# Kernel tuning notes

Hardware: AMD Instinct MI355X
Metric: run time of the kernel (lower is better)

## Reference

```python
import jax, jax.numpy as jnp
import numpy as np

# Static graph layout: 64 equal-size graphs so per-graph k is static (jit-friendly).
B = 64          # number of graphs
N_PER = 4096    # nodes per graph (batch vector is sorted, equal blocks)
N = B * N_PER   # 262144 total nodes
C = 128         # in_channels
E = 4194304     # number of edges (avg degree 16)
RATIO = 0.8
K = int(np.ceil(RATIO * N_PER))  # 3277 nodes kept per graph


def setup_inputs() -> dict:
    key = jax.random.key(0)
    k1, k2, k3 = jax.random.split(key, 3)
    x = jax.random.normal(k1, (N, C), dtype=jnp.float32)
    # learned projection (torch init is zeros; use small randn so scores are non-degenerate)
    coefficient = jax.random.normal(k2, (C, 1), dtype=jnp.float32) * 0.1
    edge_index = jax.random.randint(k3, (2, E), 0, N, dtype=jnp.int32)
    # sorted, equal-size graph assignment (matches torch_geometric batch convention)
    batch = jnp.repeat(jnp.arange(B, dtype=jnp.int32), N_PER)
    return {"x": x, "coefficient": coefficient, "edge_index": edge_index, "batch": batch}


def reference(x, coefficient, edge_index, batch):
    # score = x @ coefficient, squeezed -> [N]
    score = (x @ coefficient)[:, 0]

    # topk(): per-graph descending sort + take top ceil(ratio*n) nodes.
    # Equal-size sorted graphs -> dense view is a plain reshape; lax.top_k gives
    # descending-sorted indices per graph, matching torch's dense sort+mask path.
    dense = score.reshape(B, N_PER)              # [B, N_PER]
    _, idx = jax.lax.top_k(dense, K)             # [B, K] local indices, score-descending
    offsets = (jnp.arange(B, dtype=idx.dtype) * N_PER)[:, None]
    perm = (idx + offsets).reshape(-1)           # [B*K] global node indices

    # gather nodes, gate by sigmoid(score)
    gate = jax.nn.sigmoid(score[perm])           # [B*K]
    x_pooled = x[perm] * gate[:, None]           # [B*K, C]
    batch_pooled = batch[perm]

    # filter_adj: relabel kept nodes 0..B*K-1, drop edges with a removed endpoint.
    node_map = jnp.full((N,), -1, dtype=jnp.int32)
    node_map = node_map.at[perm].set(jnp.arange(perm.shape[0], dtype=jnp.int32))
    row = node_map[edge_index[0]]
    col = node_map[edge_index[1]]
    valid = (row >= 0) & (col >= 0)              # [E]
    # static-shape equivalent of torch's dynamic edge filtering: stable-sort valid
    # edges to the front (preserving original order), pad invalid slots with -1.
    order = jnp.argsort(jnp.logical_not(valid), stable=True)
    new_edge_index = jnp.stack([row, col])[:, order]
    new_edge_index = jnp.where(valid[order][None, :], new_edge_index, -1)

    return (x_pooled, new_edge_index, batch_pooled, perm)
```

## Files before the change

### kernel.cpp

```cpp
#include <hip/hip_runtime.h>
#include <hip/hip_bf16.h>

#define BG    64
#define NPER  4096
#define NTOT  (BG * NPER)
#define CC    128
#define EE    4194304
#define KK    3277
#define BK    (BG * KK)
#define NBLK  512
#define EPB   8192

#define OFF_X     0
#define OFF_EDGE  (BK * CC)
#define OFF_BATCH (OFF_EDGE + 2 * EE)
#define OFF_PERM  (OFF_BATCH + BK)

#define CH0_BYTES  ((size_t)OFF_EDGE * 4)
#define A_OFF_B    (CH0_BYTES - (size_t)NTOT * 4)
#define BM_OFF_B   (A_OFF_B - 32768)
#define LP_OFF_B   (BM_OFF_B - 16384)
#define BO_OFF_B   (LP_OFF_B - 8192)
#define BC_OFF_B   (LP_OFF_B - 16384)
#define CTRL_OFF_B (LP_OFF_B - 16640)
#define PAIRS_OFF_B (CTRL_OFF_B - (size_t)EE * 4)

typedef unsigned long long u64;

static __device__ __forceinline__ unsigned short bf16_bits(float f) {
    __hip_bfloat16 h = __float2bfloat16(f);
    return *reinterpret_cast<unsigned short*>(&h);
}
static __device__ __forceinline__ unsigned obf(float v) {
    return ((unsigned)bf16_bits(v)) << 16;
}
static __device__ __forceinline__ unsigned ald(const unsigned* p) {
    return __hip_atomic_load(p, __ATOMIC_ACQUIRE, __HIP_MEMORY_SCOPE_AGENT);
}
static __device__ __forceinline__ void ast(unsigned* p, unsigned v) {
    __hip_atomic_store(p, v, __ATOMIC_RELEASE, __HIP_MEMORY_SCOPE_AGENT);
}

__global__ void score_kernel(const float* __restrict__ x,
                             const float* __restrict__ coef,
                             float* __restrict__ arr_f,
                             unsigned* __restrict__ ctrl) {
    if (blockIdx.x == 0 && threadIdx.x < 2) ast(&ctrl[threadIdx.x], 0u);

    int lane = threadIdx.x & 63;
    int half = lane >> 5;
    int cg   = lane & 31;
    int waveId = (blockIdx.x * blockDim.x + threadIdx.x) >> 6;
    int nWaves = (gridDim.x * blockDim.x) >> 6;

    float4 c = ((const float4*)coef)[cg];

    for (int pair = waveId; pair < NTOT / 2; pair += nWaves) {
        int row = 2 * pair + half;
        float4 v = ((const float4*)(x + (size_t)row * CC))[cg];
        double s = (double)v.x * c.x + (double)v.y * c.y
                 + (double)v.z * c.z + (double)v.w * c.w;
        #pragma unroll
        for (int off = 16; off > 0; off >>= 1)
            s += __shfl_xor(s, off, 64);
        if (cg == 0) arr_f[row] = (float)s;
    }
}

__global__ __launch_bounds__(512) void topk_kernel(const float* __restrict__ arr_f,
                                                   unsigned* __restrict__ st_li,
                                                   unsigned* __restrict__ st_gate,
                                                   unsigned* __restrict__ bm_g,
                                                   unsigned short* __restrict__ lp_g) {
    __shared__ unsigned hist[2048];
    __shared__ unsigned sScan[512];
    __shared__ unsigned sSel[2];
    __shared__ unsigned sTie[128];
    __shared__ unsigned lbm[128];
    __shared__ unsigned lpc[128];

    int b = blockIdx.x, t = threadIdx.x;
    const float* s = arr_f + (b << 12);

    float4 v0 = *(const float4*)(s + (t << 3));
    float4 v1 = *(const float4*)(s + (t << 3) + 4);
    float vv[8] = {v0.x, v0.y, v0.z, v0.w, v1.x, v1.y, v1.z, v1.w};
    unsigned key[8];
    #pragma unroll
    for (int m = 0; m < 8; ++m) {
        unsigned u = __float_as_uint(vv[m]);
        u = u ^ ((u >> 31) ? 0xFFFFFFFFu : 0x80000000u);
        key[m] = ~u;
    }

    unsigned need = KK;

    for (int i = t; i < 2048; i += 512) hist[i] = 0;
    __syncthreads();
    #pragma unroll
    for (int m = 0; m < 8; ++m) atomicAdd(&hist[key[m] >> 21], 1u);
    __syncthreads();
    {
        unsigned c0 = hist[t*4], c1 = hist[t*4+1], c2 = hist[t*4+2], c3 = hist[t*4+3];
        unsigned s4 = c0 + c1 + c2 + c3;
        sScan[t] = s4; __syncthreads();
        #pragma unroll
        for (int off = 1; off < 512; off <<= 1) {
            unsigned add = (t >= off) ? sScan[t-off] : 0u; __syncthreads();
            sScan[t] += add; __syncthreads();
        }
        unsigned excl = sScan[t] - s4;
        if (excl < need && need <= sScan[t]) {
            unsigned cum = excl, bin = t*4u;
            if      (cum + c0 >= need)           { sSel[0]=bin;   sSel[1]=cum; }
            else if (cum + c0 + c1 >= need)      { sSel[0]=bin+1; sSel[1]=cum+c0; }
            else if (cum + c0 + c1 + c2 >= need) { sSel[0]=bin+2; sSel[1]=cum+c0+c1; }
            else                                 { sSel[0]=bin+3; sSel[1]=cum+c0+c1+c2; }
        }
        __syncthreads();
    }
    unsigned B1 = sSel[0]; need -= sSel[1];
    __syncthreads();

    for (int i = t; i < 2048; i += 512) hist[i] = 0;
    __syncthreads();
    #pragma unroll
    for (int m = 0; m < 8; ++m)
        if ((key[m] >> 21) == B1) atomicAdd(&hist[(key[m] >> 10) & 2047u], 1u);
    __syncthreads();
    {
        unsigned c0 = hist[t*4], c1 = hist[t*4+1], c2 = hist[t*4+2], c3 = hist[t*4+3];
        unsigned s4 = c0 + c1 + c2 + c3;
        sScan[t] = s4; __syncthreads();
        #pragma unroll
        for (int off = 1; off < 512; off <<= 1) {
            unsigned add = (t >= off) ? sScan[t-off] : 0u; __syncthreads();
            sScan[t] += add; __syncthreads();
        }
        unsigned excl = sScan[t] - s4;
        if (excl < need && need <= sScan[t]) {
            unsigned cum = excl, bin = t*4u;
            if      (cum + c0 >= need)           { sSel[0]=bin;   sSel[1]=cum; }
            else if (cum + c0 + c1 >= need)      { sSel[0]=bin+1; sSel[1]=cum+c0; }
            else if (cum + c0 + c1 + c2 >= need) { sSel[0]=bin+2; sSel[1]=cum+c0+c1; }
            else                                 { sSel[0]=bin+3; sSel[1]=cum+c0+c1+c2; }
        }
        __syncthreads();
    }
    unsigned B2 = sSel[0]; need -= sSel[1];
    unsigned P2 = (B1 << 11) | B2;
    __syncthreads();

    for (int i = t; i < 2048; i += 512) hist[i] = 0;
    __syncthreads();
    #pragma unroll
    for (int m = 0; m < 8; ++m)
        if ((key[m] >> 10) == P2) atomicAdd(&hist[key[m] & 1023u], 1u);
    __syncthreads();
    {
        unsigned c0 = hist[t*2], c1 = hist[t*2+1];
        unsigned s2 = c0 + c1;
        sScan[t] = s2; __syncthreads();
        #pragma unroll
        for (int off = 1; off < 512; off <<= 1) {
            unsigned add = (t >= off) ? sScan[t-off] : 0u; __syncthreads();
            sScan[t] += add; __syncthreads();
        }
        unsigned excl = sScan[t] - s2;
        if (excl < need && need <= sScan[t]) {
            if (excl + c0 >= need) { sSel[0] = t*2u;   sSel[1] = excl; }
            else                   { sSel[0] = t*2u+1; sSel[1] = excl + c0; }
        }
        __syncthreads();
    }
    unsigned KSTAR = (P2 << 10) | sSel[0];
    unsigned needT = need - sSel[1];
    __syncthreads();

    if (t < 128) sTie[t] = 0;
    __syncthreads();
    #pragma unroll
    for (int m = 0; m < 8; ++m) {
        if (key[m] == KSTAR) {
            unsigned idx = (unsigned)((t << 3) | m);
            atomicOr(&sTie[idx >> 5], 1u << (idx & 31));
        }
    }
    __syncthreads();
    if (t == 0) {
        unsigned rem = needT, it = 0;
        for (int w = 0; w < 128; ++w) {
            unsigned word = sTie[w], pc = __popc(word);
            if (rem <= pc) {
                for (unsigned bit = 0; ; ++bit)
                    if ((word >> bit) & 1u) { if (--rem == 0) { it = w*32u + bit; break; } }
                break;
            }
            rem -= pc;
        }
        sSel[0] = it;
    }
    __syncthreads();
    unsigned idxT = sSel[0];

    if (t < 128) lbm[t] = 0u;
    __syncthreads();
    unsigned kmask = 0;
    #pragma unroll
    for (int m = 0; m < 8; ++m) {
        unsigned idx = (unsigned)((t << 3) | m);
        bool kept = (key[m] < KSTAR) || (key[m] == KSTAR && idx <= idxT);
        if (kept) { kmask |= 1u << m; atomicOr(&lbm[idx >> 5], 1u << (idx & 31)); }
    }
    __syncthreads();
    if (t < 128) lpc[t] = __popc(lbm[t]);
    __syncthreads();
    #pragma unroll
    for (int off = 1; off < 128; off <<= 1) {
        unsigned add = (t < 128 && t >= off) ? lpc[t - off] : 0u;
        __syncthreads();
        if (t < 128) lpc[t] += add;
        __syncthreads();
    }
    if (t < 128) {
        unsigned w = lbm[t];
        bm_g[(b << 7) + t] = w;
        lp_g[(b << 7) + t] = (unsigned short)(lpc[t] - __popc(w));
    }
    #pragma unroll
    for (int m = 0; m < 8; ++m) {
        if ((kmask >> m) & 1u) {
            unsigned idx = (unsigned)((t << 3) | m);
            unsigned w = lbm[idx >> 5];
            unsigned p = (lpc[idx >> 5] - __popc(w))
                       + (unsigned)__popc(w & ((1u << (idx & 31)) - 1u));
            int j = b * KK + (int)p;
            float gate = 1.0f / (1.0f + expf(-vv[m]));
            st_li[j]   = idx;
            st_gate[j] = __float_as_uint(gate);
        }
    }
}

__global__ __launch_bounds__(512, 4) void edge_pass1(
        const int* __restrict__ edge,
        const unsigned* __restrict__ bm_g,
        const unsigned short* __restrict__ lp_g,
        unsigned* __restrict__ pairs,
        unsigned* __restrict__ counts,
        unsigned* __restrict__ prefix,
        unsigned* __restrict__ ctrl) {
    __shared__ unsigned sBm[8192];
    __shared__ unsigned short sLp[8192];
    __shared__ unsigned sWaveSum[8];
    __shared__ unsigned sScan[512];
    __shared__ int sTicket;

    int b = blockIdx.x;
    int base = b << 13;
    int tid = threadIdx.x;
    int lane = tid & 63, wid = tid >> 6;
    u64 lmask = (1ull << lane) - 1ull;

    {
        const uint4* bmv = (const uint4*)bm_g;
        uint4* sBmv = (uint4*)sBm;
        #pragma unroll
        for (int r = 0; r < 4; ++r) sBmv[(r << 9) + tid] = bmv[(r << 9) + tid];
        const uint4* lpv = (const uint4*)lp_g;
        uint4* sLpv = (uint4*)sLp;
        #pragma unroll
        for (int r = 0; r < 2; ++r) sLpv[(r << 9) + tid] = lpv[(r << 9) + tid];
    }
    __syncthreads();

    int chunk = base + (wid << 10);

    int ev0[16], ev1[16];
    #pragma unroll
    for (int k = 0; k < 16; ++k) ev0[k] = edge[chunk + (k << 6) + lane];
    #pragma unroll
    for (int k = 0; k < 16; ++k) ev1[k] = edge[EE + chunk + (k << 6) + lane];

    u64 bal[16];
    unsigned pk[16];
    unsigned cnt = 0;
    #pragma unroll
    for (int k = 0; k < 16; ++k) {
        int u0i = ev0[k], u1i = ev1[k];
        unsigned w0 = sBm[u0i >> 5], w1 = sBm[u1i >> 5];
        bool valid = ((w0 >> (u0i & 31)) & (w1 >> (u1i & 31)) & 1u) != 0u;
        bal[k] = __ballot(valid);
        unsigned pkk = 0;
        if (valid) {
            unsigned j0 = (unsigned)(u0i >> 12) * KK + sLp[u0i >> 5]
                        + (unsigned)__popc(w0 & ((1u << (u0i & 31)) - 1u));
            unsigned j1 = (unsigned)(u1i >> 12) * KK + sLp[u1i >> 5]
                        + (unsigned)__popc(w1 & ((1u << (u1i & 31)) - 1u));
            pkk = obf((float)j0) | (unsigned)bf16_bits((float)j1);
        }
        pk[k] = pkk;
        cnt += (unsigned)__popcll(bal[k]);
    }

    if (lane == 0) sWaveSum[wid] = cnt;
    __syncthreads();

    unsigned waveBase = 0, run = 0;
    #pragma unroll
    for (int w = 0; w < 8; ++w) {
        unsigned s = sWaveSum[w];
        if (w < wid) waveBase += s;
        run += s;
    }

    unsigned* pb = pairs + base;
    unsigned wrun = 0;
    #pragma unroll
    for (int k = 0; k < 16; ++k) {
        if ((bal[k] >> lane) & 1ull) {
            unsigned pos = waveBase + wrun + (unsigned)__popcll(bal[k] & lmask);
            pb[pos] = pk[k];
        }
        wrun += (unsigned)__popcll(bal[k]);
    }

    if (tid == 0) {
        ast(&counts[b], run);
        sTicket = (int)__hip_atomic_fetch_add(&ctrl[0], 1u, __ATOMIC_ACQ_REL,
                                              __HIP_MEMORY_SCOPE_AGENT);
    }
    __syncthreads();

    if (sTicket == NBLK - 1) {
        unsigned v = ald(&counts[tid]);
        sScan[tid] = v;
        __syncthreads();
        #pragma unroll
        for (int off = 1; off < 512; off <<= 1) {
            unsigned add = (tid >= off) ? sScan[tid - off] : 0u;
            __syncthreads();
            sScan[tid] += add;
            __syncthreads();
        }
        prefix[tid] = sScan[tid] - v;
        if (tid == 511) prefix[NBLK] = sScan[511];
    }
}

__global__ __launch_bounds__(256) void edge_pass2(
        const unsigned* __restrict__ pairs,
        const unsigned* __restrict__ prefix,
        unsigned* __restrict__ out32) {
    int b = blockIdx.x;
    unsigned base = (unsigned)(b << 13);
    unsigned tid = threadIdx.x;
    unsigned blockOff = prefix[b];
    unsigned cnt = prefix[b + 1] - blockOff;
    unsigned nvalid = prefix[NBLK];
    unsigned* oe = out32 + OFF_EDGE;
    const unsigned* pb = pairs + base;

    for (unsigned i = tid; i < cnt; i += 256u) {
        unsigned w = pb[i];
        oe[blockOff + i]      = w & 0xFFFF0000u;
        oe[EE + blockOff + i] = w << 16;
    }
    unsigned tailBase = nvalid + base - blockOff;
    unsigned tcnt = (unsigned)EPB - cnt;
    unsigned NEG1 = obf(-1.0f);
    for (unsigned i = tid; i < tcnt; i += 256u) {
        oe[tailBase + i]      = NEG1;
        oe[EE + tailBase + i] = NEG1;
    }
}

__global__ void gather_kernel(const float* __restrict__ x,
                              const unsigned* __restrict__ st_li,
                              const unsigned* __restrict__ st_gate,
                              unsigned* __restrict__ out32) {
    int tid = blockIdx.x * blockDim.x + threadIdx.x;
    int rowsPerGrid = (gridDim.x * blockDim.x) >> 5;
    int rid = tid >> 5;
    int cg  = tid & 31;

    for (int row = rid; row < BK; row += rowsPerGrid) {
        int b  = row / KK;
        int li = (int)st_li[row];
        int node = (b << 12) + li;
        float g = __uint_as_float(st_gate[row]);
        float4 v = ((const float4*)(x + (size_t)node * CC))[cg];
        uint4 o;
        o.x = obf(v.x * g);
        o.y = obf(v.y * g);
        o.z = obf(v.z * g);
        o.w = obf(v.w * g);
        ((uint4*)(out32 + OFF_X))[(size_t)row * 32 + cg] = o;
        if (cg == 0) {
            out32[OFF_BATCH + row] = obf((float)b);
            out32[OFF_PERM + row]  = obf((float)node);
        }
    }
}

extern "C" void kernel_launch(void* const* d_in, const int* in_sizes, int n_in,
                              void* d_out, int out_size, void* d_ws, size_t ws_size,
                              hipStream_t stream) {
    const float* x    = nullptr;
    const float* coef = nullptr;
    const int*   edge = nullptr;
    for (int i = 0; i < n_in; ++i) {
        switch (in_sizes[i]) {
            case NTOT * CC: x    = (const float*)d_in[i]; break;
            case CC:        coef = (const float*)d_in[i]; break;
            case 2 * EE:    edge = (const int*)d_in[i];   break;
            default: break;
        }
    }
    if (!x || !coef || !edge) return;

    char* ob = (char*)d_out;
    unsigned* out32 = (unsigned*)d_out;
    float*          A      = (float*)(ob + A_OFF_B);
    unsigned*       bm_g   = (unsigned*)(ob + BM_OFF_B);
    unsigned short* lp_g   = (unsigned short*)(ob + LP_OFF_B);
    unsigned*       counts = (unsigned*)(ob + BC_OFF_B);
    unsigned*       prefix = (unsigned*)(ob + BO_OFF_B);
    unsigned*       ctrl   = (unsigned*)(ob + CTRL_OFF_B);
    unsigned*       pairs  = (unsigned*)(ob + PAIRS_OFF_B);
    unsigned* st_li   = out32 + OFF_BATCH;
    unsigned* st_gate = out32 + OFF_PERM;

    score_kernel<<<2048, 256, 0, stream>>>(x, coef, A, ctrl);
    topk_kernel<<<BG, 512, 0, stream>>>(A, st_li, st_gate, bm_g, lp_g);
    edge_pass1<<<NBLK, 512, 0, stream>>>(edge, bm_g, lp_g, pairs, counts,
                                         prefix, ctrl);
    edge_pass2<<<NBLK, 256, 0, stream>>>(pairs, prefix, out32);
    gather_kernel<<<4096, 256, 0, stream>>>(x, st_li, st_gate, out32);
}
```

Measured before the change: 139.4 us.

## Move scratch buffers to workspace and fuse edge pass2 with gather kernel

Scratch buffers (scores, bitmaps, pairs, counts, prefix, ctrl) move from the output buffer into the workspace when it is large enough. That removes the overlap between the scratch areas and the output regions. With the overlap gone, edge_pass2 and the gather kernel become independent and are merged into one launch with disjoint block ranges, so edge compaction and row gathering run concurrently and one launch is saved. If no workspace is available, the old two-launch path is used.

```diff
diff --git a/kernel.cpp b/kernel.cpp
--- a/kernel.cpp
+++ b/kernel.cpp
@@ -24,6 +24,15 @@
 #define BC_OFF_B   (LP_OFF_B - 16384)
 #define CTRL_OFF_B (LP_OFF_B - 16640)
 #define PAIRS_OFF_B (CTRL_OFF_B - (size_t)EE * 4)
+
+#define WS_PAIRS_B  ((size_t)0)
+#define WS_A_B      ((size_t)EE * 4)
+#define WS_BM_B     (WS_A_B + (size_t)NTOT * 4)
+#define WS_LP_B     (WS_BM_B + 32768)
+#define WS_BC_B     (WS_LP_B + 16384)
+#define WS_BO_B     (WS_BC_B + 2048)
+#define WS_CTRL_B   (WS_BO_B + 2064)
+#define WS_NEEDED   (WS_CTRL_B + 16)
 
 typedef unsigned long long u64;
 
@@ -348,13 +357,12 @@
     }
 }
 
-__global__ __launch_bounds__(256) void edge_pass2(
+static __device__ __forceinline__ void pass2_body(
+        int b, unsigned tid,
         const unsigned* __restrict__ pairs,
         const unsigned* __restrict__ prefix,
         unsigned* __restrict__ out32) {
-    int b = blockIdx.x;
     unsigned base = (unsigned)(b << 13);
-    unsigned tid = threadIdx.x;
     unsigned blockOff = prefix[b];
     unsigned cnt = prefix[b + 1] - blockOff;
     unsigned nvalid = prefix[NBLK];
@@ -375,14 +383,14 @@
     }
 }
 
-__global__ void gather_kernel(const float* __restrict__ x,
-                              const unsigned* __restrict__ st_li,
-                              const unsigned* __restrict__ st_gate,
-                              unsigned* __restrict__ out32) {
-    int tid = blockIdx.x * blockDim.x + threadIdx.x;
-    int rowsPerGrid = (gridDim.x * blockDim.x) >> 5;
-    int rid = tid >> 5;
-    int cg  = tid & 31;
+static __device__ __forceinline__ void gather_body(
+        int gtid, int rowsPerGrid,
+        const float* __restrict__ x,
+        const unsigned* __restrict__ st_li,
+        const unsigned* __restrict__ st_gate,
+        unsigned* __restrict__ out32) {
+    int rid = gtid >> 5;
+    int cg  = gtid & 31;
 
     for (int row = rid; row < BK; row += rowsPerGrid) {
         int b  = row / KK;
@@ -403,6 +411,36 @@
     }
 }
 
+__global__ __launch_bounds__(256) void fused_p2_gather(
+        const unsigned* __restrict__ pairs,
+        const unsigned* __restrict__ prefix,
+        const float* __restrict__ x,
+        const unsigned* __restrict__ st_li,
+        const unsigned* __restrict__ st_gate,
+        unsigned* __restrict__ out32) {
+    if (blockIdx.x < NBLK) {
+        pass2_body(blockIdx.x, threadIdx.x, pairs, prefix, out32);
+    } else {
+        int gtid = (blockIdx.x - NBLK) * 256 + threadIdx.x;
+        gather_body(gtid, (4096 * 256) >> 5, x, st_li, st_gate, out32);
+    }
+}
+
+__global__ __launch_bounds__(256) void edge_pass2(
+        const unsigned* __restrict__ pairs,
+        const unsigned* __restrict__ prefix,
+        unsigned* __restrict__ out32) {
+    pass2_body(blockIdx.x, threadIdx.x, pairs, prefix, out32);
+}
+
+__global__ void gather_kernel(const float* __restrict__ x,
+                              const unsigned* __restrict__ st_li,
+                              const unsigned* __restrict__ st_gate,
+                              unsigned* __restrict__ out32) {
+    int gtid = blockIdx.x * blockDim.x + threadIdx.x;
+    gather_body(gtid, (int)((gridDim.x * blockDim.x) >> 5), x, st_li, st_gate, out32);
+}
+
 extern "C" void kernel_launch(void* const* d_in, const int* in_sizes, int n_in,
                               void* d_out, int out_size, void* d_ws, size_t ws_size,
                               hipStream_t stream) {
@@ -419,22 +457,30 @@
     }
     if (!x || !coef || !edge) return;
 
-    char* ob = (char*)d_out;
     unsigned* out32 = (unsigned*)d_out;
-    float*          A      = (float*)(ob + A_OFF_B);
-    unsigned*       bm_g   = (unsigned*)(ob + BM_OFF_B);
-    unsigned short* lp_g   = (unsigned short*)(ob + LP_OFF_B);
-    unsigned*       counts = (unsigned*)(ob + BC_OFF_B);
-    unsigned*       prefix = (unsigned*)(ob + BO_OFF_B);
-    unsigned*       ctrl   = (unsigned*)(ob + CTRL_OFF_B);
-    unsigned*       pairs  = (unsigned*)(ob + PAIRS_OFF_B);
     unsigned* st_li   = out32 + OFF_BATCH;
     unsigned* st_gate = out32 + OFF_PERM;
+
+    bool useWs = (d_ws != nullptr) && (ws_size >= WS_NEEDED);
+    char* sb = useWs ? (char*)d_ws : (char*)d_out;
+
+    float*          A      = (float*)(sb + (useWs ? WS_A_B    : A_OFF_B));
+    unsigned*       bm_g   = (unsigned*)(sb + (useWs ? WS_BM_B   : BM_OFF_B));
+    unsigned short* lp_g   = (unsigned short*)(sb + (useWs ? WS_LP_B : LP_OFF_B));
+    unsigned*       counts = (unsigned*)(sb + (useWs ? WS_BC_B   : BC_OFF_B));
+    unsigned*       prefix = (unsigned*)(sb + (useWs ? WS_BO_B   : BO_OFF_B));
+    unsigned*       ctrl   = (unsigned*)(sb + (useWs ? WS_CTRL_B : CTRL_OFF_B));
+    unsigned*       pairs  = (unsigned*)(sb + (useWs ? WS_PAIRS_B : PAIRS_OFF_B));
 
     score_kernel<<<2048, 256, 0, stream>>>(x, coef, A, ctrl);
     topk_kernel<<<BG, 512, 0, stream>>>(A, st_li, st_gate, bm_g, lp_g);
     edge_pass1<<<NBLK, 512, 0, stream>>>(edge, bm_g, lp_g, pairs, counts,
                                          prefix, ctrl);
-    edge_pass2<<<NBLK, 256, 0, stream>>>(pairs, prefix, out32);
-    gather_kernel<<<4096, 256, 0, stream>>>(x, st_li, st_gate, out32);
-}
+    if (useWs) {
+        fused_p2_gather<<<NBLK + 4096, 256, 0, stream>>>(pairs, prefix, x,
+                                                         st_li, st_gate, out32);
+    } else {
+        edge_pass2<<<NBLK, 256, 0, stream>>>(pairs, prefix, out32);
+        gather_kernel<<<4096, 256, 0, stream>>>(x, st_li, st_gate, out32);
+    }
+}
```

New measurement: 139.4 us, median of 2. Within noise of the previous version (-0.0%).
